# Optimization experiments

Hardware: AMD Instinct MI355X
Metric: run time of the kernel (lower is better)

Reference implementation:

```python
import jax, jax.numpy as jnp
import numpy as np

HEADS = 16
KV_HEADS = 8
DIMS = 64
IN_DIMS = 1024
B, S = 2, 2048


def rope(x):
    # RoPE applied over the FULL flattened last dim (heads*dims), as in the source.
    seq_len, dim = x.shape[-2], x.shape[-1]
    thetas = 1.0 / 10000 ** (jnp.arange(0, dim, 2) / dim)          # [dim/2]
    ang = jnp.arange(1, seq_len + 1)[:, None] * thetas[None, :]    # [S, dim/2] (positions start at 1)
    cos, sin = jnp.cos(ang), jnp.sin(ang)
    xe, xo = x[..., ::2], x[..., 1::2]
    real = xe * cos - xo * sin
    imag = xe * sin + xo * cos
    return jnp.stack([real, imag], axis=-1).reshape(x.shape)


def setup_inputs() -> dict:
    key = jax.random.key(0)
    k1, k2, k3, k4, k5 = jax.random.split(key, 5)
    q = jax.random.normal(k1, (B, S, IN_DIMS), dtype=jnp.float32)
    sd = 1.0 / np.sqrt(IN_DIMS)
    Wq = jax.random.normal(k2, (IN_DIMS, HEADS * DIMS), dtype=jnp.float32) * sd
    Wk = jax.random.normal(k3, (IN_DIMS, KV_HEADS * DIMS), dtype=jnp.float32) * sd
    Wv = jax.random.normal(k4, (IN_DIMS, KV_HEADS * DIMS), dtype=jnp.float32) * sd
    Wo = jax.random.normal(k5, (HEADS * DIMS, IN_DIMS), dtype=jnp.float32) / np.sqrt(HEADS * DIMS)
    return {"q": q, "Wq": Wq, "Wk": Wk, "Wv": Wv, "Wo": Wo}


def reference(q, Wq, Wk, Wv, Wo):
    batch, seq_len, in_dims = q.shape
    kv = q  # self-attention (kv=None path)
    xq = rope(q @ Wq)            # [B, S, H*D], RoPE over flattened dim
    xk = rope(kv @ Wk)           # [B, S, Hk*D]
    xv = kv @ Wv                 # [B, S, Hk*D]
    # element-wise repeat(2) on last axis, exactly as source (interleaved duplication)
    xk = jnp.repeat(xk, 2, axis=-1)   # [B, S, H*D]
    xv = jnp.repeat(xv, 2, axis=-1)
    xq = xq.reshape(batch, seq_len, HEADS, DIMS).transpose(0, 2, 1, 3)  # [B,H,S,D]
    xk = xk.reshape(batch, seq_len, HEADS, DIMS).transpose(0, 2, 3, 1)  # [B,H,D,S]
    xv = xv.reshape(batch, seq_len, HEADS, DIMS).transpose(0, 2, 1, 3)  # [B,H,S,D]
    scale = (DIMS / HEADS) ** (-0.5)  # source uses dims/heads, not 1/sqrt(dims)
    scores = jax.nn.softmax((xq @ xk) * scale, axis=-1)  # [B,H,S,S]
    out = (scores @ xv).transpose(0, 2, 1, 3).reshape(batch, seq_len, -1)
    return out @ Wo
```

## Files before the change

kernel.cpp:

```cpp
#include <hip/hip_runtime.h>
#include <hip/hip_bf16.h>
#include <math.h>

#define HEADS 16
#define KV_HEADS 8
#define DIMS 64
#define IN_DIMS 1024
#define BATCH 2
#define SEQ 2048

typedef __attribute__((ext_vector_type(8))) short short8;
typedef __attribute__((ext_vector_type(4))) float f32x4;
typedef __attribute__((ext_vector_type(4))) unsigned int u32x4;

__device__ __forceinline__ short f2bf(float f) {
    __hip_bfloat16 h = __float2bfloat16(f);
    return *reinterpret_cast<short*>(&h);
}

__device__ __forceinline__ float e2(float x) {
    return __builtin_amdgcn_exp2f(x);
}

__device__ __forceinline__ unsigned int cvtpk(float a, float b) {
    unsigned int r;
    asm("v_cvt_pk_bf16_f32 %0, %1, %2" : "=v"(r) : "v"(a), "v"(b));
    return r;
}

__device__ __forceinline__ void gl_lds16(const void* g, void* l) {
    __builtin_amdgcn_global_load_lds(
        (const __attribute__((address_space(1))) unsigned int*)g,
        (__attribute__((address_space(3))) unsigned int*)l, 16, 0, 0);
}

#define LOG2_10000 13.287712379549449f
#define LOG2_2PI   2.6514961294723187f
#define CSCALE (0.5f * 1.4426950408889634f)

__device__ __forceinline__ void sincos_rev(float ang_rev, float* sn, float* cs) {
    float fr = ang_rev - floorf(ang_rev);
    *sn = __builtin_amdgcn_sinf(fr);
    *cs = __builtin_amdgcn_cosf(fr);
}

__global__ __launch_bounds__(256) void prep_weights(
    const float* __restrict__ Wq, const float* __restrict__ Wk,
    const float* __restrict__ Wv, const float* __restrict__ Wo,
    short* __restrict__ WT, short* __restrict__ WoPt,
    const float* __restrict__ qin, short* __restrict__ Abf)
{
    __shared__ float t[32][33];
    int z = blockIdx.z;
    if (z >= 4) {
        int i = (z - 4) * 1024 + blockIdx.y * 32 + blockIdx.x;
        size_t idx = ((size_t)i * 256 + threadIdx.x) * 8;
        float4 a = *(const float4*)(qin + idx);
        float4 c = *(const float4*)(qin + idx + 4);
        u32x4 s = { cvtpk(a.x, a.y), cvtpk(a.z, a.w),
                    cvtpk(c.x, c.y), cvtpk(c.z, c.w) };
        *(u32x4*)(Abf + idx) = s;
        return;
    }
    int bx = blockIdx.x * 32, by = blockIdx.y * 32;
    int x = threadIdx.x & 31, y = threadIdx.x >> 5;
    if (z == 3) {
        if (by >= 512) return;
        #pragma unroll
        for (int i = 0; i < 32; i += 8) {
            int d = by + y + i;
            t[y + i][x] = Wo[(size_t)(2 * d) * 1024 + bx + x]
                        + Wo[(size_t)(2 * d + 1) * 1024 + bx + x];
        }
        __syncthreads();
        #pragma unroll
        for (int i = 0; i < 32; i += 8)
            WoPt[(size_t)(bx + y + i) * 512 + by + x] = f2bf(t[x][y + i]);
    } else {
        const float* W = (z == 0) ? Wq : ((z == 1) ? Wk : Wv);
        int N = (z == 0) ? 1024 : 512;
        if (bx >= N) return;
        short* dst = WT + ((z == 0) ? 0 : ((z == 1) ? (size_t)1024 * 1024
                                                    : (size_t)1536 * 1024));
        #pragma unroll
        for (int i = 0; i < 32; i += 8)
            t[y + i][x] = W[(size_t)(by + y + i) * N + bx + x];
        __syncthreads();
        #pragma unroll
        for (int i = 0; i < 32; i += 8)
            dst[(size_t)(bx + y + i) * 1024 + by + x] = f2bf(t[x][y + i]);
    }
}

__global__ __launch_bounds__(256) void gemm_qkv(
    const short* __restrict__ A, const short* __restrict__ Bt,
    short* __restrict__ Qp, short* __restrict__ Kb, short* __restrict__ Vtg)
{
    const int K = 1024;
    __shared__ short As[128][64];
    __shared__ short Bs[128][64];

    int tid  = threadIdx.x;
    int lane = tid & 63, wave = tid >> 6;
    int quad = lane >> 4, ln = lane & 15;
    int wm = (wave >> 1) * 64, wn = (wave & 1) * 64;
    int row0 = blockIdx.y * 128, col0 = blockIdx.x * 128;

    int sr = lane >> 3;
    int sk = (lane & 7) * 8;

    f32x4 acc[4][4] = {};

    for (int kt = 0; kt < K; kt += 64) {
        #pragma unroll
        for (int u = 0; u < 4; ++u) {
            int r = wave * 32 + u * 8;
            gl_lds16(A + (size_t)(row0 + r + sr) * K + kt + sk, &As[r][0]);
        }
        #pragma unroll
        for (int u = 0; u < 4; ++u) {
            int r = wave * 32 + u * 8;
            gl_lds16(Bt + (size_t)(col0 + r + sr) * K + kt + sk, &Bs[r][0]);
        }
        __syncthreads();

        #pragma unroll
        for (int k0 = 0; k0 < 64; k0 += 32) {
            short8 af[4], bfr[4];
            #pragma unroll
            for (int i = 0; i < 4; ++i)
                af[i] = *(const short8*)&As[wm + 16 * i + ln][k0 + quad * 8];
            #pragma unroll
            for (int j = 0; j < 4; ++j)
                bfr[j] = *(const short8*)&Bs[wn + 16 * j + ln][k0 + quad * 8];
            #pragma unroll
            for (int i = 0; i < 4; ++i)
                #pragma unroll
                for (int j = 0; j < 4; ++j)
                    acc[i][j] = __builtin_amdgcn_mfma_f32_16x16x32_bf16(
                        af[i], bfr[j], acc[i][j], 0, 0, 0);
        }
        __syncthreads();
    }

    bool evn = (lane & 1) == 0;

    if (col0 < 1024) {
        #pragma unroll
        for (int j = 0; j < 4; ++j) {
            int col = col0 + wn + 16 * j + ln;
            float tr = e2(-(float)(col & ~1) / 1024.f * LOG2_10000 - LOG2_2PI);
            #pragma unroll
            for (int i = 0; i < 4; ++i)
                #pragma unroll
                for (int r = 0; r < 4; ++r) {
                    int row = row0 + wm + 16 * i + quad * 4 + r;
                    float xe = acc[i][j][r];
                    float xo = __shfl_xor(xe, 1);
                    float sn, cs;
                    sincos_rev((float)((row & (SEQ - 1)) + 1) * tr, &sn, &cs);
                    float o = (xe * (cs + sn) + xo * (cs - sn)) * CSCALE;
                    if (evn)
                        Qp[(size_t)row * 512 + (col >> 1)] = f2bf(o);
                }
        }
    } else if (col0 < 1536) {
        #pragma unroll
        for (int j = 0; j < 4; ++j) {
            int c = col0 + wn + 16 * j + ln - 1024;
            float tr = e2(-(float)(c & ~1) / 512.f * LOG2_10000 - LOG2_2PI);
            #pragma unroll
            for (int i = 0; i < 4; ++i)
                #pragma unroll
                for (int r = 0; r < 4; ++r) {
                    int row = row0 + wm + 16 * i + quad * 4 + r;
                    float xe = acc[i][j][r];
                    float xo = __shfl_xor(xe, 1);
                    float sn, cs;
                    sincos_rev((float)((row & (SEQ - 1)) + 1) * tr, &sn, &cs);
                    unsigned int o = cvtpk(xe * cs - xo * sn, xe * sn + xo * cs);
                    if (evn)
                        *(unsigned int*)(Kb + (size_t)row * 512 + c) = o;
                }
        }
    } else {
        int b = row0 >> 11;
        int s0 = (row0 & (SEQ - 1)) + wm + quad * 4;
        #pragma unroll
        for (int j = 0; j < 4; ++j) {
            int dim = col0 + wn + 16 * j + ln - 1536;
            short* dst = Vtg + ((size_t)(b * 512 + dim)) * SEQ + s0;
            #pragma unroll
            for (int i = 0; i < 4; ++i) {
                short4 o4 = { f2bf(acc[i][j][0]), f2bf(acc[i][j][1]),
                              f2bf(acc[i][j][2]), f2bf(acc[i][j][3]) };
                *(short4*)(dst + 16 * i) = o4;
            }
        }
    }
}

__global__ __launch_bounds__(512) void flash_attn(
    const short* __restrict__ Qp, const short* __restrict__ Kb,
    const short* __restrict__ Vtg, short* __restrict__ AO32)
{
    __shared__ short Qs[128][40];
    __shared__ short Ks[2][64][40];
    __shared__ short Vt[2][32][72];

    int tid = threadIdx.x;
    int qt = blockIdx.x & 15;
    int h  = (blockIdx.x >> 4) & 15;
    int b  = blockIdx.x >> 8;

    int lane = tid & 63, wave = tid >> 6;
    int quad = lane >> 4, ln = lane & 15;
    int qw = wave * 16;

    {
        int row = tid >> 2, off = (tid & 3) * 8;
        *(short8*)&Qs[row][off] =
            *(const short8*)(Qp + (size_t)(b * SEQ + qt * 128 + row) * 512 + h * 32 + off);
    }

    const short* Kgb = Kb + (size_t)(b * SEQ) * 512 + 32 * h;
    const short* Vgb = Vtg + ((size_t)b * 512 + 32 * h) * SEQ;

    bool doK = tid < 256;
    int st = tid & 255;
    int krow = st >> 2, koff = (st & 3) * 8;
    int prow = ((krow >> 5) << 5) | (((krow >> 2) & 1) << 4)
             | (((krow >> 3) & 3) << 2) | (krow & 3);
    int vrow = st >> 3, voff = (st & 7) * 8;

    short8 sreg;
    if (doK) {
        sreg = *(const short8*)(Kgb + (size_t)krow * 512 + koff);
        *(short8*)&Ks[0][prow][koff] = sreg;
    } else {
        sreg = *(const short8*)(Vgb + (size_t)vrow * SEQ + voff);
        *(short8*)&Vt[0][vrow][voff] = sreg;
    }
    __syncthreads();

    short8 af = *(const short8*)&Qs[qw + ln][quad * 8];

    float lsum = 0.f;
    f32x4 Oacc[2] = {};
    const f32x4 zz = {};

    for (int t = 0; t < 32; ++t) {
        int cur = t & 1;

        if (t < 31) {
            int ktn = (t + 1) * 64;
            if (doK)
                sreg = *(const short8*)(Kgb + (size_t)(ktn + krow) * 512 + koff);
            else
                sreg = *(const short8*)(Vgb + (size_t)vrow * SEQ + ktn + voff);
        }

        f32x4 sc[4];
        __builtin_amdgcn_s_setprio(1);
        #pragma unroll
        for (int j0 = 0; j0 < 4; ++j0) {
            short8 kf = *(const short8*)&Ks[cur][j0 * 16 + ln][quad * 8];
            sc[j0] = __builtin_amdgcn_mfma_f32_16x16x32_bf16(kf, af, zz, 0, 0, 0);
        }
        __builtin_amdgcn_s_setprio(0);

        short8 pf[2];
        #pragma unroll
        for (int kg = 0; kg < 2; ++kg) {
            float p0 = e2(sc[2 * kg][0]);
            float p1 = e2(sc[2 * kg][1]);
            float p2 = e2(sc[2 * kg][2]);
            float p3 = e2(sc[2 * kg][3]);
            float p4 = e2(sc[2 * kg + 1][0]);
            float p5 = e2(sc[2 * kg + 1][1]);
            float p6 = e2(sc[2 * kg + 1][2]);
            float p7 = e2(sc[2 * kg + 1][3]);
            lsum += ((p0 + p1) + (p2 + p3)) + ((p4 + p5) + (p6 + p7));
            short8 s = { f2bf(p0), f2bf(p1), f2bf(p2), f2bf(p3),
                         f2bf(p4), f2bf(p5), f2bf(p6), f2bf(p7) };
            pf[kg] = s;
        }

        __builtin_amdgcn_s_setprio(1);
        #pragma unroll
        for (int kg = 0; kg < 2; ++kg) {
            #pragma unroll
            for (int ng = 0; ng < 2; ++ng) {
                short8 vf = *(const short8*)&Vt[cur][ng * 16 + ln][kg * 32 + quad * 8];
                Oacc[ng] = __builtin_amdgcn_mfma_f32_16x16x32_bf16(
                    vf, pf[kg], Oacc[ng], 0, 0, 0);
            }
        }
        __builtin_amdgcn_s_setprio(0);

        if (t < 31) {
            if (doK) *(short8*)&Ks[cur ^ 1][prow][koff] = sreg;
            else     *(short8*)&Vt[cur ^ 1][vrow][voff] = sreg;
        }
        __syncthreads();
    }

    lsum += __shfl_xor(lsum, 16);
    lsum += __shfl_xor(lsum, 32);
    float inv = 1.f / lsum;

    size_t row = (size_t)(b * SEQ) + qt * 128 + qw + ln;
    #pragma unroll
    for (int ng = 0; ng < 2; ++ng) {
        short4 o4 = { f2bf(Oacc[ng][0] * inv), f2bf(Oacc[ng][1] * inv),
                      f2bf(Oacc[ng][2] * inv), f2bf(Oacc[ng][3] * inv) };
        *(short4*)&AO32[row * 512 + h * 32 + ng * 16 + quad * 4] = o4;
    }
}

__global__ __launch_bounds__(256) void gemm_wo(
    const short* __restrict__ A, const short* __restrict__ Bt,
    float* __restrict__ C)
{
    __shared__ short As[64][64];
    __shared__ short Bs[128][64];

    int tid  = threadIdx.x;
    int lane = tid & 63, wave = tid >> 6;
    int quad = lane >> 4, ln = lane & 15;
    int wm = (wave >> 1) * 32, wn = (wave & 1) * 64;
    int row0 = blockIdx.y * 64, col0 = blockIdx.x * 128;
    const int K = 512, N = 1024;

    int sr = lane >> 3;
    int sk = (lane & 7) * 8;

    f32x4 acc[2][4] = {};

    for (int kt = 0; kt < K; kt += 64) {
        #pragma unroll
        for (int u = 0; u < 2; ++u) {
            int r = wave * 16 + u * 8;
            gl_lds16(A + (size_t)(row0 + r + sr) * K + kt + sk, &As[r][0]);
        }
        #pragma unroll
        for (int u = 0; u < 4; ++u) {
            int r = wave * 32 + u * 8;
            gl_lds16(Bt + (size_t)(col0 + r + sr) * K + kt + sk, &Bs[r][0]);
        }
        __syncthreads();

        #pragma unroll
        for (int k0 = 0; k0 < 64; k0 += 32) {
            short8 af[2], bfr[4];
            #pragma unroll
            for (int i = 0; i < 2; ++i)
                af[i] = *(const short8*)&As[wm + 16 * i + ln][k0 + quad * 8];
            #pragma unroll
            for (int j = 0; j < 4; ++j)
                bfr[j] = *(const short8*)&Bs[wn + 16 * j + ln][k0 + quad * 8];
            #pragma unroll
            for (int i = 0; i < 2; ++i)
                #pragma unroll
                for (int j = 0; j < 4; ++j)
                    acc[i][j] = __builtin_amdgcn_mfma_f32_16x16x32_bf16(
                        af[i], bfr[j], acc[i][j], 0, 0, 0);
        }
        __syncthreads();
    }

    #pragma unroll
    for (int i = 0; i < 2; ++i)
        #pragma unroll
        for (int j = 0; j < 4; ++j)
            #pragma unroll
            for (int r = 0; r < 4; ++r)
                C[(size_t)(row0 + wm + 16 * i + quad * 4 + r) * N
                  + col0 + wn + 16 * j + ln] = acc[i][j][r];
}

extern "C" void kernel_launch(void* const* d_in, const int* in_sizes, int n_in,
                              void* d_out, int out_size, void* d_ws, size_t ws_size,
                              hipStream_t stream)
{
    const float* q  = (const float*)d_in[0];
    const float* Wq = (const float*)d_in[1];
    const float* Wk = (const float*)d_in[2];
    const float* Wv = (const float*)d_in[3];
    const float* Wo = (const float*)d_in[4];
    float* out = (float*)d_out;

    const int M = BATCH * SEQ;

    short* Abf  = (short*)d_ws;
    short* WT   = (short*)((float*)d_ws + (size_t)M * 2048);
    short* WoPt = WT + (size_t)2048 * 1024;
    short* Qp   = WoPt + (size_t)1024 * 512;
    short* Kb   = Qp + (size_t)M * 512;
    short* Vtg  = Kb + (size_t)M * 512;
    short* AO32 = WT;

    dim3 blk(256);

    prep_weights<<<dim3(32, 32, 6), blk, 0, stream>>>(Wq, Wk, Wv, Wo, WT, WoPt, q, Abf);

    gemm_qkv<<<dim3(16, 32), blk, 0, stream>>>(Abf, WT, Qp, Kb, Vtg);

    flash_attn<<<BATCH * HEADS * (SEQ / 128), dim3(512), 0, stream>>>(Qp, Kb, Vtg, AO32);

    gemm_wo<<<dim3(8, 64), blk, 0, stream>>>(AO32, WoPt, out);
}
```

Baseline: 171.7 us.

## Permute Q/K weight columns so RoPE pairs land in one lane

The weight-transpose prep kernel now permutes the output columns of Wq and Wk within each 64-column group, so the even and odd RoPE partners sit in the same lane across adjacent MFMA tiles instead of in neighbouring lanes. The QKV GEMM epilogue then reads both partners from its own accumulators, drops the cross-lane shuffle and the even-lane predicate, and computes sincos only once per pair rather than redundantly in both lanes. The cost is a more intricate index mapping that must stay consistent between the prep kernel and the epilogue.

```diff
diff --git a/kernel.cpp b/kernel.cpp
--- a/kernel.cpp
+++ b/kernel.cpp
@@ -87,8 +87,16 @@
             t[y + i][x] = W[(size_t)(by + y + i) * N + bx + x];
         __syncthreads();
         #pragma unroll
-        for (int i = 0; i < 32; i += 8)
-            dst[(size_t)(bx + y + i) * 1024 + by + x] = f2bf(t[x][y + i]);
+        for (int i = 0; i < 32; i += 8) {
+            int c = bx + y + i;
+            int g = c;
+            if (z <= 1) {
+                int oc = c & 63;
+                g = (c & ~63) | (((oc & 1) | ((oc >> 5) << 1)) << 4)
+                              | ((oc & 31) >> 1);
+            }
+            dst[(size_t)g * 1024 + by + x] = f2bf(t[x][y + i]);
+        }
     }
 }
 
@@ -143,45 +151,45 @@
         __syncthreads();
     }
 
-    bool evn = (lane & 1) == 0;
-
     if (col0 < 1024) {
-        #pragma unroll
-        for (int j = 0; j < 4; ++j) {
-            int col = col0 + wn + 16 * j + ln;
-            float tr = e2(-(float)(col & ~1) / 1024.f * LOG2_10000 - LOG2_2PI);
-            #pragma unroll
-            for (int i = 0; i < 4; ++i)
+        int ubase = (col0 + wn) >> 1;
+        #pragma unroll
+        for (int jp = 0; jp < 2; ++jp) {
+            int u = ubase + jp * 16 + ln;
+            float tr = e2(-(float)u / 512.f * LOG2_10000 - LOG2_2PI);
+            #pragma unroll
+            for (int i = 0; i < 4; ++i) {
+                int rowb = row0 + wm + 16 * i + quad * 4;
                 #pragma unroll
                 for (int r = 0; r < 4; ++r) {
-                    int row = row0 + wm + 16 * i + quad * 4 + r;
-                    float xe = acc[i][j][r];
-                    float xo = __shfl_xor(xe, 1);
+                    int row = rowb + r;
                     float sn, cs;
                     sincos_rev((float)((row & (SEQ - 1)) + 1) * tr, &sn, &cs);
-                    float o = (xe * (cs + sn) + xo * (cs - sn)) * CSCALE;
-                    if (evn)
-                        Qp[(size_t)row * 512 + (col >> 1)] = f2bf(o);
+                    float xe = acc[i][2 * jp][r], xo = acc[i][2 * jp + 1][r];
+                    Qp[(size_t)row * 512 + u] =
+                        f2bf((xe * (cs + sn) + xo * (cs - sn)) * CSCALE);
                 }
+            }
         }
     } else if (col0 < 1536) {
-        #pragma unroll
-        for (int j = 0; j < 4; ++j) {
-            int c = col0 + wn + 16 * j + ln - 1024;
-            float tr = e2(-(float)(c & ~1) / 512.f * LOG2_10000 - LOG2_2PI);
-            #pragma unroll
-            for (int i = 0; i < 4; ++i)
+        int pbase = (col0 - 1024 + wn) >> 1;
+        #pragma unroll
+        for (int jp = 0; jp < 2; ++jp) {
+            int p = pbase + jp * 16 + ln;
+            float tr = e2(-(float)p / 256.f * LOG2_10000 - LOG2_2PI);
+            #pragma unroll
+            for (int i = 0; i < 4; ++i) {
+                int rowb = row0 + wm + 16 * i + quad * 4;
                 #pragma unroll
                 for (int r = 0; r < 4; ++r) {
-                    int row = row0 + wm + 16 * i + quad * 4 + r;
-                    float xe = acc[i][j][r];
-                    float xo = __shfl_xor(xe, 1);
+                    int row = rowb + r;
                     float sn, cs;
                     sincos_rev((float)((row & (SEQ - 1)) + 1) * tr, &sn, &cs);
-                    unsigned int o = cvtpk(xe * cs - xo * sn, xe * sn + xo * cs);
-                    if (evn)
-                        *(unsigned int*)(Kb + (size_t)row * 512 + c) = o;
+                    float xe = acc[i][2 * jp][r], xo = acc[i][2 * jp + 1][r];
+                    *(unsigned int*)(Kb + (size_t)row * 512 + 2 * p) =
+                        cvtpk(xe * cs - xo * sn, xe * sn + xo * cs);
                 }
+            }
         }
     } else {
         int b = row0 >> 11;
```

Result: faster. 149.7 us (-12.9%).
